# Optimization experiments

Hardware: AMD Instinct MI355X
Metric: run time of the kernel (lower is better)

The kernel has to match this reference:

```python
import jax, jax.numpy as jnp
import numpy as np

N, D, K = 8192, 128, 30  # num_nodes, isize, k


def setup_inputs() -> dict:
    key = jax.random.key(0)
    k1, k2, k3 = jax.random.split(key, 3)
    features = jax.random.normal(k1, (N, D), dtype=jnp.float32)
    # module initializes layers to identity; perturb slightly so weights matter
    eye = jnp.eye(D, dtype=jnp.float32)
    W1 = eye + 0.02 * jax.random.normal(k2, (D, D), dtype=jnp.float32)
    W2 = eye + 0.02 * jax.random.normal(k3, (D, D), dtype=jnp.float32)
    b1 = jnp.zeros((D,), dtype=jnp.float32)
    b2 = jnp.zeros((D,), dtype=jnp.float32)
    return {"features": features, "W1": W1, "b1": b1, "W2": W2, "b2": b2, "kp1": K + 1}


def reference(features, W1, b1, W2, b2, kp1):
    # internal_forward: Linear -> ReLU -> Linear (act='relu', last layer no act)
    h = jax.nn.relu(features @ W1.T + b1)
    emb = h @ W2.T + b2
    # F.normalize(dim=1, p=2)
    emb = emb / jnp.clip(jnp.linalg.norm(emb, axis=1, keepdims=True), 1e-12, None)
    # cal_similarity_graph: dense cosine similarity [N, N]
    sim = emb @ emb.T
    # top_k: keep top (k+1) entries per row, zero the rest
    _, idx = jax.lax.top_k(sim, kp1)  # idx: [N, kp1]
    mask = jnp.zeros_like(sim).at[jnp.arange(sim.shape[0])[:, None], idx].set(1.0)
    sparse_graph = sim * mask
    # apply_non_linearity('relu', i): elementwise relu
    return jax.nn.relu(sparse_graph)
```

## Files before the change

kernel.cpp:

```cpp
#include <hip/hip_runtime.h>
#include <hip/hip_fp16.h>

#define NN 8192
#define DDIM 128
#define DELTA 0.010f
#define MAXC 256
#define SIMSTRIDE 16384

typedef short short8 __attribute__((ext_vector_type(8)));
typedef unsigned short ushort8 __attribute__((ext_vector_type(8)));
typedef float f32x16 __attribute__((ext_vector_type(16)));

__device__ __forceinline__ ushort bf16_rne(float v) {
    const unsigned x = __float_as_uint(v);
    return (ushort)((x + 0x7FFFu + ((x >> 16) & 1u)) >> 16);
}

__global__ __launch_bounds__(128, 1)
void mlp_norm_kernel(const float* __restrict__ X, const float* __restrict__ W1,
                     const float* __restrict__ b1, const float* __restrict__ W2,
                     const float* __restrict__ b2, float* __restrict__ emb,
                     ushort* __restrict__ ebh, int rowsPerBlock)
{
    const int t = threadIdx.x;
    float4 w1r[32], w2r[32];
#pragma unroll
    for (int i = 0; i < 32; ++i) w1r[i] = *(const float4*)&W1[t * DDIM + i * 4];
#pragma unroll
    for (int i = 0; i < 32; ++i) w2r[i] = *(const float4*)&W2[t * DDIM + i * 4];
    const float bb1 = b1[t], bb2 = b2[t];

    __shared__ float sx[DDIM];
    __shared__ float sh[DDIM];
    __shared__ float wred[2];

    const int row0 = blockIdx.x * rowsPerBlock;
    for (int r = 0; r < rowsPerBlock; ++r) {
        const int row = row0 + r;
        sx[t] = X[(size_t)row * DDIM + t];
        __syncthreads();
        float acc = bb1;
#pragma unroll
        for (int i = 0; i < 32; ++i) {
            const float4 xv = *(const float4*)&sx[i * 4];
            acc = fmaf(xv.x, w1r[i].x, acc);
            acc = fmaf(xv.y, w1r[i].y, acc);
            acc = fmaf(xv.z, w1r[i].z, acc);
            acc = fmaf(xv.w, w1r[i].w, acc);
        }
        sh[t] = fmaxf(acc, 0.f);
        __syncthreads();
        float acc2 = bb2;
#pragma unroll
        for (int i = 0; i < 32; ++i) {
            const float4 hv = *(const float4*)&sh[i * 4];
            acc2 = fmaf(hv.x, w2r[i].x, acc2);
            acc2 = fmaf(hv.y, w2r[i].y, acc2);
            acc2 = fmaf(hv.z, w2r[i].z, acc2);
            acc2 = fmaf(hv.w, w2r[i].w, acc2);
        }
        float sq = acc2 * acc2;
#pragma unroll
        for (int off = 1; off < 64; off <<= 1) sq += __shfl_xor(sq, off);
        if ((t & 63) == 0) wred[t >> 6] = sq;
        __syncthreads();
        const float ss = wred[0] + wred[1];
        const float inv = 1.0f / fmaxf(sqrtf(ss), 1e-12f);
        const float v = acc2 * inv;
        emb[(size_t)row * DDIM + t] = v;
        ebh[(size_t)row * DDIM + t] = bf16_rne(v);
        __syncthreads();
    }
}

__global__ __launch_bounds__(256)
void simgemm_bf16(const ushort* __restrict__ ebh, ushort* __restrict__ sim)
{
    __shared__ ushort lA[128 * 128];
    __shared__ ushort lB[128 * 128];

    const int tid = threadIdx.x;
    const int bi = blockIdx.x & 63, bj = blockIdx.x >> 6;
    const int m0 = bi << 7, n0 = bj << 7;
    const int lane = tid & 63, wid = tid >> 6;
    const int wr = wid >> 1, wc = wid & 1;
    const int frow = lane & 31, fsel = lane >> 5;

    const int srow0 = tid >> 4, sg = tid & 15;
#pragma unroll
    for (int i = 0; i < 8; ++i) {
        const int row = srow0 + i * 16;
        const int so = row * 128 + ((sg ^ (row & 15)) << 3);
        *(uint4*)&lA[so] = *(const uint4*)&ebh[(size_t)(m0 + row) * DDIM + sg * 8];
        *(uint4*)&lB[so] = *(const uint4*)&ebh[(size_t)(n0 + row) * DDIM + sg * 8];
    }
    __syncthreads();

    f32x16 acc[2][2];
#pragma unroll
    for (int mb = 0; mb < 2; ++mb)
#pragma unroll
        for (int nb = 0; nb < 2; ++nb)
#pragma unroll
            for (int q = 0; q < 16; ++q) acc[mb][nb][q] = 0.f;

#pragma unroll
    for (int ks = 0; ks < 8; ++ks) {
        const int g = ks * 2 + fsel;
        short8 av[2], bv[2];
#pragma unroll
        for (int mb = 0; mb < 2; ++mb) {
            const int r = wr * 64 + mb * 32 + frow;
            av[mb] = *(const short8*)&lA[r * 128 + ((g ^ (r & 15)) << 3)];
        }
#pragma unroll
        for (int nb = 0; nb < 2; ++nb) {
            const int r = wc * 64 + nb * 32 + frow;
            bv[nb] = *(const short8*)&lB[r * 128 + ((g ^ (r & 15)) << 3)];
        }
#pragma unroll
        for (int mb = 0; mb < 2; ++mb)
#pragma unroll
            for (int nb = 0; nb < 2; ++nb)
                acc[mb][nb] = __builtin_amdgcn_mfma_f32_32x32x16_bf16(
                    av[mb], bv[nb], acc[mb][nb], 0, 0, 0);
    }

#pragma unroll
    for (int mb = 0; mb < 2; ++mb)
#pragma unroll
        for (int nb = 0; nb < 2; ++nb)
#pragma unroll
            for (int q = 0; q < 16; ++q) {
                const int rl = (q & 3) + 8 * (q >> 2) + 4 * fsel;
                const int grow = m0 + wr * 64 + mb * 32 + rl;
                const int gcol = n0 + wc * 64 + nb * 32 + (lane & 31);
                sim[(size_t)grow * SIMSTRIDE + gcol] =
                    __half_as_ushort(__float2half_rn(acc[mb][nb][q]));
            }
}

__global__ __launch_bounds__(256)
void topk_relu_kernel(float* __restrict__ out, const float* __restrict__ emb,
                      const int* __restrict__ kp1p)
{
    const int row = blockIdx.x;
    const int t = threadIdx.x;
    const int w = t >> 6;
    const int lane = t & 63;
    const unsigned kp1 = (unsigned)kp1p[0];
    const ushort* simrow = (const ushort*)out + (size_t)row * SIMSTRIDE;
    float* rowp = out + (size_t)row * NN;

    __shared__ unsigned bitmap[NN / 32];
    __shared__ float semb[DDIM];
    __shared__ unsigned hist[4][256];
    __shared__ unsigned h2[64];
    __shared__ unsigned wpart[4];
    __shared__ unsigned sBA[4];
    __shared__ int cidx[MAXC];
    __shared__ float cval[MAXC];
    __shared__ int cnum;

    bitmap[t] = 0;
    hist[0][t] = 0; hist[1][t] = 0; hist[2][t] = 0; hist[3][t] = 0;
    if (t < 64) h2[t] = 0;
    if (t < 4) sBA[t] = 0;
    if (t == 0) cnum = 0;
    if (t < DDIM) semb[t] = emb[(size_t)row * DDIM + t];
    __syncthreads();

    unsigned u[32];
#pragma unroll
    for (int i = 0; i < 4; ++i) {
        const ushort8 v8 = *(const ushort8*)&simrow[i * 2048 + t * 8];
#pragma unroll
        for (int j = 0; j < 8; ++j) {
            const unsigned uu = (v8[j] < 0x8000u) ? (unsigned)v8[j] : 0u;
            u[i * 8 + j] = uu;
            if (uu) atomicAdd(&hist[w][uu >> 6], 1u);
        }
    }
    __syncthreads();

    const unsigned tot = hist[0][t] + hist[1][t] + hist[2][t] + hist[3][t];
    unsigned s = tot;
#pragma unroll
    for (int off = 1; off < 64; off <<= 1) {
        const unsigned o = __shfl_down(s, off);
        if (lane + off < 64) s += o;
    }
    if (lane == 0) wpart[w] = s;
    __syncthreads();
    unsigned addhi = 0;
    for (int w2 = w + 1; w2 < 4; ++w2) addhi += wpart[w2];
    const unsigned S = s + addhi;
    if (S >= kp1 && S - tot < kp1) { sBA[0] = (unsigned)t; sBA[1] = S - tot; }
    if (t == 0 && wpart[0] + wpart[1] + wpart[2] + wpart[3] < kp1) sBA[3] = 1u;
    __syncthreads();

    const bool keepall = (sBA[3] != 0u);
    if (!keepall) {
        const unsigned binB = sBA[0];
#pragma unroll
        for (int q = 0; q < 32; ++q)
            if (u[q] && (u[q] >> 6) == binB) atomicAdd(&h2[u[q] & 63u], 1u);
        __syncthreads();
        if (t < 64) {
            const unsigned need = kp1 - sBA[1];
            const unsigned h = h2[t];
            unsigned s2 = h;
#pragma unroll
            for (int off = 1; off < 64; off <<= 1) {
                const unsigned o = __shfl_down(s2, off);
                if (t + off < 64) s2 += o;
            }
            if (s2 >= need && s2 - h < need) sBA[2] = (binB << 6) | (unsigned)t;
        }
        __syncthreads();
    }

    unsigned hi16, lo16;
    if (!keepall) {
        const unsigned teff = sBA[2];
        const float Treal = __half2float(__ushort_as_half((ushort)teff));
        hi16 = (unsigned)__half_as_ushort(__float2half_rn(Treal + DELTA)) + 1u;
        const float loR = Treal - DELTA;
        if (loR <= 0.f) lo16 = 1u;
        else {
            const unsigned l = __half_as_ushort(__float2half_rn(loR));
            lo16 = (l > 1u) ? l - 1u : 1u;
        }

        unsigned acnt = 0;
#pragma unroll
        for (int q = 0; q < 32; ++q) {
            const unsigned uu = u[q];
            if (uu > hi16) ++acnt;
            else if (uu >= lo16) {
                const int p = atomicAdd(&cnum, 1);
                if (p < MAXC) cidx[p] = (q >> 3) * 2048 + t * 8 + (q & 7);
            }
        }
#pragma unroll
        for (int off = 1; off < 64; off <<= 1) acnt += __shfl_xor(acnt, off);
        if (lane == 0) wpart[w] = acnt;
        __syncthreads();
        const unsigned A = wpart[0] + wpart[1] + wpart[2] + wpart[3];
        const int nc = cnum < MAXC ? cnum : MAXC;

        if (t < nc) {
            const float* rb = emb + (size_t)cidx[t] * DDIM;
            float a = 0.f;
#pragma unroll 8
            for (int k = 0; k < DDIM; ++k) a = fmaf(semb[k], rb[k], a);
            cval[t] = a;
        }
        __syncthreads();
        if (t < nc) {
            const float e = cval[t];
            const int my = cidx[t];
            int r = 0;
            for (int d = 0; d < nc; ++d)
                r += (cval[d] > e) || (cval[d] == e && cidx[d] < my);
            if (A + (unsigned)r < kp1)
                atomicOr(&bitmap[my >> 5], 1u << (my & 31));
        }
        __syncthreads();
    } else {
        hi16 = 0u;
        lo16 = 0xFFFFu;
        __syncthreads();
    }

#pragma unroll
    for (int i = 0; i < 4; ++i) {
        const int col0 = i * 2048 + t * 8;
        float o[8];
#pragma unroll
        for (int j = 0; j < 8; ++j) {
            const unsigned uu = u[i * 8 + j];
            const int idx = col0 + j;
            const bool keep = (uu > hi16) ||
                              (uu >= lo16 &&
                               ((bitmap[idx >> 5] >> (idx & 31)) & 1u));
            o[j] = keep ? __half2float(__ushort_as_half((ushort)uu)) : 0.f;
        }
        *(float4*)&rowp[col0]     = make_float4(o[0], o[1], o[2], o[3]);
        *(float4*)&rowp[col0 + 4] = make_float4(o[4], o[5], o[6], o[7]);
    }
}

extern "C" void kernel_launch(void* const* d_in, const int* in_sizes, int n_in,
                              void* d_out, int out_size, void* d_ws, size_t ws_size,
                              hipStream_t stream)
{
    const float* X  = (const float*)d_in[0];
    const float* W1 = (const float*)d_in[1];
    const float* b1 = (const float*)d_in[2];
    const float* W2 = (const float*)d_in[3];
    const float* b2 = (const float*)d_in[4];
    const int* kp1  = (const int*)d_in[5];
    float* out = (float*)d_out;
    float* emb  = (float*)d_ws;
    ushort* ebh = (ushort*)((char*)d_ws + (size_t)NN * DDIM * 4);

    mlp_norm_kernel<<<512, 128, 0, stream>>>(X, W1, b1, W2, b2, emb, ebh, 16);
    simgemm_bf16<<<4096, 256, 0, stream>>>(ebh, (ushort*)out);
    topk_relu_kernel<<<NN, 256, 0, stream>>>(out, emb, kp1);
}
```

Before: 202.7 us.

## Stage sim tile through LDS for coalesced stores; drop second-level top-k histogram

```diff
diff --git a/kernel.cpp b/kernel.cpp
--- a/kernel.cpp
+++ b/kernel.cpp
@@ -126,18 +126,28 @@
                     av[mb], bv[nb], acc[mb][nb], 0, 0, 0);
     }
 
+    __syncthreads();
 #pragma unroll
     for (int mb = 0; mb < 2; ++mb)
 #pragma unroll
-        for (int nb = 0; nb < 2; ++nb)
+        for (int nb = 0; nb < 2; ++nb) {
+            const int cl = wc * 64 + nb * 32 + (lane & 31);
 #pragma unroll
             for (int q = 0; q < 16; ++q) {
-                const int rl = (q & 3) + 8 * (q >> 2) + 4 * fsel;
-                const int grow = m0 + wr * 64 + mb * 32 + rl;
-                const int gcol = n0 + wc * 64 + nb * 32 + (lane & 31);
-                sim[(size_t)grow * SIMSTRIDE + gcol] =
-                    __half_as_ushort(__float2half_rn(acc[mb][nb][q]));
+                const int rl = wr * 64 + mb * 32 + (q & 3) + 8 * (q >> 2) + 4 * fsel;
+                lA[rl * 128 + cl] = __half_as_ushort(__float2half_rn(acc[mb][nb][q]));
             }
+        }
+    __syncthreads();
+    {
+        const int rr0 = tid >> 4, cc = (tid & 15) * 8;
+#pragma unroll
+        for (int i = 0; i < 8; ++i) {
+            const int row = rr0 + i * 16;
+            *(uint4*)&sim[(size_t)(m0 + row) * SIMSTRIDE + n0 + cc] =
+                *(const uint4*)&lA[row * 128 + cc];
+        }
+    }
 }
 
 __global__ __launch_bounds__(256)
@@ -155,17 +165,14 @@
     __shared__ unsigned bitmap[NN / 32];
     __shared__ float semb[DDIM];
     __shared__ unsigned hist[4][256];
-    __shared__ unsigned h2[64];
     __shared__ unsigned wpart[4];
-    __shared__ unsigned sBA[4];
+    __shared__ unsigned sHL[2];
     __shared__ int cidx[MAXC];
     __shared__ float cval[MAXC];
     __shared__ int cnum;
 
     bitmap[t] = 0;
     hist[0][t] = 0; hist[1][t] = 0; hist[2][t] = 0; hist[3][t] = 0;
-    if (t < 64) h2[t] = 0;
-    if (t < 4) sBA[t] = 0;
     if (t == 0) cnum = 0;
     if (t < DDIM) semb[t] = emb[(size_t)row * DDIM + t];
     __syncthreads();
@@ -195,43 +202,26 @@
     unsigned addhi = 0;
     for (int w2 = w + 1; w2 < 4; ++w2) addhi += wpart[w2];
     const unsigned S = s + addhi;
-    if (S >= kp1 && S - tot < kp1) { sBA[0] = (unsigned)t; sBA[1] = S - tot; }
-    if (t == 0 && wpart[0] + wpart[1] + wpart[2] + wpart[3] < kp1) sBA[3] = 1u;
-    __syncthreads();
-
-    const bool keepall = (sBA[3] != 0u);
-    if (!keepall) {
-        const unsigned binB = sBA[0];
-#pragma unroll
-        for (int q = 0; q < 32; ++q)
-            if (u[q] && (u[q] >> 6) == binB) atomicAdd(&h2[u[q] & 63u], 1u);
-        __syncthreads();
-        if (t < 64) {
-            const unsigned need = kp1 - sBA[1];
-            const unsigned h = h2[t];
-            unsigned s2 = h;
-#pragma unroll
-            for (int off = 1; off < 64; off <<= 1) {
-                const unsigned o = __shfl_down(s2, off);
-                if (t + off < 64) s2 += o;
-            }
-            if (s2 >= need && s2 - h < need) sBA[2] = (binB << 6) | (unsigned)t;
-        }
-        __syncthreads();
-    }
-
-    unsigned hi16, lo16;
-    if (!keepall) {
-        const unsigned teff = sBA[2];
-        const float Treal = __half2float(__ushort_as_half((ushort)teff));
-        hi16 = (unsigned)__half_as_ushort(__float2half_rn(Treal + DELTA)) + 1u;
-        const float loR = Treal - DELTA;
-        if (loR <= 0.f) lo16 = 1u;
-        else {
-            const unsigned l = __half_as_ushort(__float2half_rn(loR));
-            lo16 = (l > 1u) ? l - 1u : 1u;
-        }
-
+    if (t == 0 && wpart[0] + wpart[1] + wpart[2] + wpart[3] < kp1) {
+        sHL[0] = 0u; sHL[1] = 0xFFFFFFFFu;
+    }
+    if (S >= kp1 && S - tot < kp1) {
+        const unsigned B = (unsigned)t;
+        const float L = __half2float(__ushort_as_half((ushort)(B << 6)));
+        const float H = __half2float(__ushort_as_half((ushort)((B << 6) | 63u)));
+        const unsigned hi =
+            (unsigned)__half_as_ushort(__float2half_rn(H + DELTA)) + 1u;
+        const float lof = L - DELTA;
+        unsigned lo;
+        if (lof <= 0.f) lo = 1u;
+        else { const unsigned l2 = __half_as_ushort(__float2half_rn(lof));
+               lo = (l2 > 1u) ? l2 - 1u : 1u; }
+        sHL[0] = hi; sHL[1] = lo;
+    }
+    __syncthreads();
+
+    const unsigned hi16 = sHL[0], lo16 = sHL[1];
+    if (hi16 != 0u) {
         unsigned acnt = 0;
 #pragma unroll
         for (int q = 0; q < 32; ++q) {
@@ -268,8 +258,6 @@
         }
         __syncthreads();
     } else {
-        hi16 = 0u;
-        lo16 = 0xFFFFu;
         __syncthreads();
     }
 
```

After: 221.3 us. +9.2%, slower.
